# Performance work log

Measured on AMD Instinct MI355X. Metric: run time of the kernel, lower is better.

Reference implementation:

```python
import jax, jax.numpy as jnp
import numpy as np
import math

B, S, D, H, WIDTH, NHW = 8, 1024, 512, 8, 8, 2
DK = D // H
S2 = S + 2 * WIDTH


def setup_inputs() -> dict:
    key = jax.random.key(0)
    ks = jax.random.split(key, 12)
    sc = 1.0 / math.sqrt(D)
    return {
        "x": jax.random.normal(ks[0], (B, S, D), jnp.float32),
        "l_attn_W": jax.random.normal(ks[1], (4, D, D), jnp.float32) * sc,  # q,k,v,out
        "l_attn_b": jnp.zeros((4, D), jnp.float32),
        "r_attn_W": jax.random.normal(ks[2], (4, D, D), jnp.float32) * sc,
        "r_attn_b": jnp.zeros((4, D), jnp.float32),
        "left_pad": jax.random.normal(ks[3], (WIDTH, D), jnp.float32) * sc,
        "right_pad": jax.random.normal(ks[4], (WIDTH, D), jnp.float32) * sc,
        "left_w": jax.random.normal(ks[5], (WIDTH + 1,), jnp.float32),
        "right_w": jax.random.normal(ks[6], (WIDTH + 1,), jnp.float32),
        "l_hw_W": jax.random.normal(ks[7], (NHW, D, 2 * D), jnp.float32) * sc,
        "l_hw_b": jnp.zeros((NHW, 2 * D), jnp.float32),
        "r_hw_W": jax.random.normal(ks[8], (NHW, D, 2 * D), jnp.float32) * sc,
        "r_hw_b": jnp.zeros((NHW, 2 * D), jnp.float32),
    }


def _mha(x, W, b, mask):
    # x: [B, S2, D]; W: [4, D, D]; mask: [1, S2, S2] bool (True = keep)
    q = (x @ W[0] + b[0]).reshape(B, S2, H, DK)
    k = (x @ W[1] + b[1]).reshape(B, S2, H, DK)
    v = (x @ W[2] + b[2]).reshape(B, S2, H, DK)
    scores = jnp.einsum('bihd,bjhd->bhij', q, k) / math.sqrt(DK)
    scores = jnp.where(mask[:, None], scores, jnp.float32(-1e9))
    p = jax.nn.softmax(scores, axis=-1)
    o = jnp.einsum('bhij,bjhd->bihd', p, v).reshape(B, S2, D)
    return o @ W[3] + b[3]


def _highway(x, Ws, bs):
    # AllenNLP-style Highway: projected -> [nonlinear | gate]
    for i in range(NHW):
        proj = x @ Ws[i] + bs[i]
        nl = jax.nn.relu(proj[..., :D])
        g = jax.nn.sigmoid(proj[..., D:])
        x = g * x + (1.0 - g) * nl
    return x


def reference(x, l_attn_W, l_attn_b, r_attn_W, r_attn_b, left_pad, right_pad,
              left_w, right_w, l_hw_W, l_hw_b, r_hw_W, r_hw_b):
    new_in = jnp.concatenate([
        jnp.broadcast_to(left_pad, (B, WIDTH, D)), x,
        jnp.broadcast_to(right_pad, (B, WIDTH, D))], axis=1)  # [B, S2, D]
    idx = jnp.arange(S2)
    diff = idx[:, None] - idx[None, :]
    lmask = ((diff >= 0) & (diff <= WIDTH + 1))[None]          # attend to [i-width-1, i]
    rmask = ((diff <= 0) & (diff >= -(WIDTH + 1)))[None]       # attend to [i, i+width+1]
    nl_attn = _mha(new_in, l_attn_W, l_attn_b, lmask)
    nr_attn = _mha(new_in, r_attn_W, r_attn_b, rmask)
    left_out = nl_attn[:, WIDTH:WIDTH + S, :]   # position end = start + width
    right_out = nr_attn[:, WIDTH:WIDTH + S, :]
    # relative-position weighted sliding windows (vectorized over all steps)
    lrel = sum(left_w[j] * new_in[:, j:j + S, :] for j in range(WIDTH + 1))
    rrel = sum(right_w[j] * new_in[:, WIDTH + j:WIDTH + j + S, :] for j in range(WIDTH + 1))
    left_out = _highway(left_out + lrel, l_hw_W, l_hw_b)
    right_out = _highway(right_out + rrel, r_hw_W, r_hw_b)
    out = jnp.concatenate([left_out, right_out], axis=-1)  # [B, S, 2D]
    return out[None]  # [1, B, S, 2D] matching torch stack layout
```

## Files before the change

kernel.cpp:

```cpp
#include <hip/hip_runtime.h>


#define B_ 8
#define S_ 1024
#define D_ 512
#define H_ 8
#define DK_ 64
#define WIDTH_ 8
#define S2_ 1040
#define NHW_ 2

typedef short bf16x8 __attribute__((ext_vector_type(8)));
typedef float f32x4 __attribute__((ext_vector_type(4)));

__device__ __forceinline__ float us2f(unsigned short u) {
  union { unsigned int i; float f; } c; c.i = ((unsigned int)u) << 16; return c.f;
}
__device__ __forceinline__ unsigned short f2us(float f) {
  union { float f; unsigned int i; } c; c.f = f;
  unsigned int x = c.i;
  return (unsigned short)((x + 0x7fffu + ((x >> 16) & 1u)) >> 16);
}
__device__ __forceinline__ unsigned int pack2(float a, float b) {
  return (unsigned int)f2us(a) | ((unsigned int)f2us(b) << 16);
}
__device__ __forceinline__ void async16(const void* g, void* l) {
  __builtin_amdgcn_global_load_lds(
      (const __attribute__((address_space(1))) void*)g,
      (__attribute__((address_space(3))) void*)l, 16, 0, 0);
}
__device__ __forceinline__ void unpack8(uint4 u, float* f) {
  unsigned int w[4] = {u.x, u.y, u.z, u.w};
  #pragma unroll
  for (int c = 0; c < 4; ++c) {
    union { unsigned int i; float g; } lo, hi;
    lo.i = w[c] << 16;
    hi.i = w[c] & 0xffff0000u;
    f[2 * c] = lo.g;
    f[2 * c + 1] = hi.g;
  }
}

__global__ __launch_bounds__(256) void k_prep(
    const float* __restrict__ x,
    const float* __restrict__ lpad, const float* __restrict__ rpad,
    const float* __restrict__ lW, const float* __restrict__ rW,
    const float* __restrict__ lb, const float* __restrict__ rb,
    const float* __restrict__ lhwW, const float* __restrict__ rhwW,
    unsigned short* __restrict__ WTall, unsigned short* __restrict__ WTp,
    unsigned short* __restrict__ hWT,
    unsigned short* __restrict__ nin, float* __restrict__ qkvbias)
{
  __shared__ float tile[32][33];
  const size_t DD = (size_t)D_ * D_;
  int bx = blockIdx.x;
  int tx = threadIdx.x & 31, ty = threadIdx.x >> 5;

  if (bx < 2048) {
    int sl = bx >> 8, rem = bx & 255;
    int side = sl >> 2, slice = sl & 3;
    int c0 = (rem & 15) * 32, r0 = (rem >> 4) * 32;
    const float* src = (side ? rW : lW) + (size_t)slice * DD;
    unsigned short* dst = (slice < 3) ? WTall + (size_t)(side * 3 + slice) * DD
                                      : WTp + (size_t)side * DD;
    #pragma unroll
    for (int i = 0; i < 4; ++i)
      tile[ty + i * 8][tx] = src[(size_t)(r0 + ty + i * 8) * D_ + c0 + tx];
    __syncthreads();
    #pragma unroll
    for (int i = 0; i < 4; ++i)
      dst[(size_t)(c0 + ty + i * 8) * D_ + r0 + tx] = f2us(tile[tx][ty + i * 8]);
    return;
  }
  if (bx < 4096) {
    int idx = bx - 2048;
    int sl = idx >> 9, rem = idx & 511;
    int c0 = (rem & 31) * 32, r0 = (rem >> 5) * 32;
    const float* src = ((sl >> 1) ? rhwW : lhwW) + (size_t)(sl & 1) * 512 * 1024;
    unsigned short* dst = hWT + (size_t)sl * 1024 * 512;
    #pragma unroll
    for (int i = 0; i < 4; ++i)
      tile[ty + i * 8][tx] = src[(size_t)(r0 + ty + i * 8) * 1024 + c0 + tx];
    __syncthreads();
    #pragma unroll
    for (int i = 0; i < 4; ++i) {
      int c = c0 + ty + i * 8;
      int q = (2 * ((c & 511) >> 4) + (c >= 512 ? 1 : 0)) * 16 + (c & 15);
      dst[(size_t)q * 512 + r0 + tx] = f2us(tile[tx][ty + i * 8]);
    }
    return;
  }
  int gid = (bx - 4096) * 256 + threadIdx.x;
  const int NTH = B_ * S2_ * 64;
  if (gid >= NTH) {
    int t = gid - NTH;
    if (t < 1536) qkvbias[t] = lb[t];
    else if (t < 3072) qkvbias[t] = rb[t - 1536];
    return;
  }
  int c8 = (gid & 63) << 3;
  int row = gid >> 6;
  int b = row / S2_;
  int t = row - b * S2_;
  const float* src;
  if (t < WIDTH_)            src = lpad + (size_t)t * D_ + c8;
  else if (t >= S_ + WIDTH_) src = rpad + (size_t)(t - S_ - WIDTH_) * D_ + c8;
  else                       src = x + ((size_t)b * S_ + (t - WIDTH_)) * D_ + c8;
  float4 a = *reinterpret_cast<const float4*>(src);
  float4 c = *reinterpret_cast<const float4*>(src + 4);
  uint4 o;
  o.x = pack2(a.x, a.y); o.y = pack2(a.z, a.w);
  o.z = pack2(c.x, c.y); o.w = pack2(c.z, c.w);
  *reinterpret_cast<uint4*>(nin + (size_t)row * D_ + c8) = o;
}

__global__ __launch_bounds__(256) void k_gemm_mfma(
    const unsigned short* __restrict__ A,
    const unsigned short* __restrict__ BT,
    const float* __restrict__ bias,
    unsigned short* __restrict__ C,
    int M, int N, int K)
{
  __shared__ unsigned short As[128 * 64];
  __shared__ unsigned short Bs[128 * 64];

  const int tid = threadIdx.x;
  const int w = tid >> 6;
  const int l = tid & 63;
  const int bm = blockIdx.y * 128;
  const int bn = blockIdx.x * 128;
  const int wrow = (w >> 1) * 64;
  const int wcol = (w & 1) * 64;

  const int lr = l >> 3;
  const int sk = (((l & 7) ^ lr) & 7) * 8;
  const unsigned short* Ap = A + (size_t)(bm + w * 8 + lr) * K + sk;
  const unsigned short* Bp = BT + (size_t)(bn + w * 8 + lr) * K + sk;
  unsigned short* lA = &As[w * 512];
  unsigned short* lB = &Bs[w * 512];
  const size_t K32 = (size_t)32 * K;

  const int fl = l & 15;
  const int fq = l >> 4;
  const int fx = fl & 7;

  f32x4 acc[4][4];
  #pragma unroll
  for (int mi = 0; mi < 4; ++mi)
    #pragma unroll
    for (int ni = 0; ni < 4; ++ni) acc[mi][ni] = (f32x4){0.f, 0.f, 0.f, 0.f};

  for (int k0 = 0; k0 < K; k0 += 64) {
    #pragma unroll
    for (int r = 0; r < 4; ++r) {
      async16(Ap + k0 + r * K32, lA + r * 2048);
      async16(Bp + k0 + r * K32, lB + r * 2048);
    }
    __syncthreads();
    #pragma unroll
    for (int s = 0; s < 2; ++s) {
      bf16x8 af[4], bfr[4];
      #pragma unroll
      for (int mi = 0; mi < 4; ++mi)
        af[mi] = *reinterpret_cast<const bf16x8*>(
            &As[(wrow + mi * 16 + fl) * 64 + (((s * 4 + fq) ^ fx) * 8)]);
      #pragma unroll
      for (int ni = 0; ni < 4; ++ni)
        bfr[ni] = *reinterpret_cast<const bf16x8*>(
            &Bs[(wcol + ni * 16 + fl) * 64 + (((s * 4 + fq) ^ fx) * 8)]);
      #pragma unroll
      for (int mi = 0; mi < 4; ++mi)
        #pragma unroll
        for (int ni = 0; ni < 4; ++ni)
          acc[mi][ni] = __builtin_amdgcn_mfma_f32_16x16x32_bf16(
              af[mi], bfr[ni], acc[mi][ni], 0, 0, 0);
    }
    __syncthreads();
  }

  float bv[4];
  #pragma unroll
  for (int ni = 0; ni < 4; ++ni) bv[ni] = bias[bn + wcol + ni * 16 + fl];

  const int rbase = (l >> 4) * 4;
  #pragma unroll
  for (int mi = 0; mi < 4; ++mi) {
    #pragma unroll
    for (int r = 0; r < 4; ++r) {
      int row = bm + wrow + mi * 16 + rbase + r;
      unsigned short* Cp = C + (size_t)row * N + bn + wcol + fl;
      #pragma unroll
      for (int ni = 0; ni < 4; ++ni)
        Cp[ni * 16] = f2us(acc[mi][ni][r] + bv[ni]);
    }
  }
}

__global__ __launch_bounds__(256) void k_gemm_proj(
    const unsigned short* __restrict__ ctx,
    const unsigned short* __restrict__ WTp,
    const unsigned short* __restrict__ nin,
    const float* __restrict__ lb3, const float* __restrict__ rb3,
    const float* __restrict__ wrel0, const float* __restrict__ wrel1,
    unsigned short* __restrict__ hwx)
{
  __shared__ unsigned short smem[128 * 136];
  unsigned short* As = smem;
  unsigned short* Bs = smem + 8192;
  const int K = 512, N = 512;
  const size_t MS = (size_t)B_ * S_ * D_;

  const int z = blockIdx.z;
  const unsigned short* A = ctx + (size_t)z * MS;
  const unsigned short* BT = WTp + (size_t)z * 512 * 512;
  const float* bias = z ? rb3 : lb3;
  const float* wrel = z ? wrel1 : wrel0;
  const int off = z * WIDTH_;

  const int tid = threadIdx.x;
  const int w = tid >> 6;
  const int l = tid & 63;
  const int bm = blockIdx.y * 128;
  const int bn = blockIdx.x * 128;
  const int wrow = (w >> 1) * 64;
  const int wcol = (w & 1) * 64;

  const int lr = l >> 3;
  const int sk = (((l & 7) ^ lr) & 7) * 8;
  const unsigned short* Ap = A + (size_t)(bm + w * 8 + lr) * K + sk;
  const unsigned short* Bp = BT + (size_t)(bn + w * 8 + lr) * K + sk;
  unsigned short* lA = &As[w * 512];
  unsigned short* lB = &Bs[w * 512];
  const size_t K32 = (size_t)32 * K;

  const int fl = l & 15;
  const int fq = l >> 4;
  const int fx = fl & 7;

  f32x4 acc[4][4];
  #pragma unroll
  for (int mi = 0; mi < 4; ++mi)
    #pragma unroll
    for (int ni = 0; ni < 4; ++ni) acc[mi][ni] = (f32x4){0.f, 0.f, 0.f, 0.f};

  for (int k0 = 0; k0 < K; k0 += 64) {
    #pragma unroll
    for (int r = 0; r < 4; ++r) {
      async16(Ap + k0 + r * K32, lA + r * 2048);
      async16(Bp + k0 + r * K32, lB + r * 2048);
    }
    __syncthreads();
    #pragma unroll
    for (int s = 0; s < 2; ++s) {
      bf16x8 af[4], bfr[4];
      #pragma unroll
      for (int mi = 0; mi < 4; ++mi)
        af[mi] = *reinterpret_cast<const bf16x8*>(
            &As[(wrow + mi * 16 + fl) * 64 + (((s * 4 + fq) ^ fx) * 8)]);
      #pragma unroll
      for (int ni = 0; ni < 4; ++ni)
        bfr[ni] = *reinterpret_cast<const bf16x8*>(
            &Bs[(wcol + ni * 16 + fl) * 64 + (((s * 4 + fq) ^ fx) * 8)]);
      #pragma unroll
      for (int mi = 0; mi < 4; ++mi)
        #pragma unroll
        for (int ni = 0; ni < 4; ++ni)
          acc[mi][ni] = __builtin_amdgcn_mfma_f32_16x16x32_bf16(
              af[mi], bfr[ni], acc[mi][ni], 0, 0, 0);
    }
    __syncthreads();
  }

  float bv[4];
  #pragma unroll
  for (int ni = 0; ni < 4; ++ni) bv[ni] = bias[bn + wcol + ni * 16 + fl];
  const int rbase = (l >> 4) * 4;
  #pragma unroll
  for (int mi = 0; mi < 4; ++mi)
    #pragma unroll
    for (int r = 0; r < 4; ++r)
      #pragma unroll
      for (int ni = 0; ni < 4; ++ni)
        smem[(wrow + mi * 16 + rbase + r) * 136 + wcol + ni * 16 + fl] =
            f2us(acc[mi][ni][r] + bv[ni]);
  __syncthreads();

  const int trow = tid >> 4;
  const int tcol = (tid & 15) * 8;
  const float w0 = wrel[0], w1 = wrel[1], w2 = wrel[2], w3 = wrel[3],
              w4 = wrel[4], w5 = wrel[5], w6 = wrel[6], w7 = wrel[7],
              w8 = wrel[8];
  const float wj[9] = {w0, w1, w2, w3, w4, w5, w6, w7, w8};
  #pragma unroll
  for (int i = 0; i < 8; ++i) {
    int r = trow + i * 16;
    int gr = bm + r;
    int b = gr >> 10, s = gr & (S_ - 1);
    float a8[8];
    unpack8(*reinterpret_cast<const uint4*>(&smem[r * 136 + tcol]), a8);
    const unsigned short* np =
        nin + ((size_t)b * S2_ + off + s) * D_ + bn + tcol;
    #pragma unroll
    for (int j = 0; j < 9; ++j) {
      float nf[8];
      unpack8(*reinterpret_cast<const uint4*>(np + (size_t)j * D_), nf);
      #pragma unroll
      for (int e = 0; e < 8; ++e) a8[e] += wj[j] * nf[e];
    }
    uint4 o;
    o.x = pack2(a8[0], a8[1]); o.y = pack2(a8[2], a8[3]);
    o.z = pack2(a8[4], a8[5]); o.w = pack2(a8[6], a8[7]);
    *reinterpret_cast<uint4*>(
        hwx + (size_t)z * MS + (size_t)gr * D_ + bn + tcol) = o;
  }
}

template <bool FINAL>
__global__ __launch_bounds__(256) void k_gemm_hw(
    const unsigned short* __restrict__ Xsrc,
    const unsigned short* __restrict__ BT, size_t bStrZ,
    const float* __restrict__ bias0, const float* __restrict__ bias1,
    unsigned short* __restrict__ Obf,
    float* __restrict__ Ofp)
{
  __shared__ unsigned short As[128 * 64];
  __shared__ unsigned short Bs[128 * 64];
  const int K = 512;
  const size_t MS = (size_t)B_ * S_ * D_;

  const int z = blockIdx.z;
  const unsigned short* A = Xsrc + (size_t)z * MS;
  BT += (size_t)z * bStrZ;
  const float* bias = z ? bias1 : bias0;

  const int tid = threadIdx.x;
  const int w = tid >> 6;
  const int l = tid & 63;
  const int bm = blockIdx.y * 128;
  const int bn = blockIdx.x * 128;
  const int wrow = (w >> 1) * 64;
  const int wcol = (w & 1) * 64;

  const int lr = l >> 3;
  const int sk = (((l & 7) ^ lr) & 7) * 8;
  const unsigned short* Ap = A + (size_t)(bm + w * 8 + lr) * K + sk;
  const unsigned short* Bp = BT + (size_t)(bn + w * 8 + lr) * K + sk;
  unsigned short* lA = &As[w * 512];
  unsigned short* lB = &Bs[w * 512];
  const size_t K32 = (size_t)32 * K;

  const int fl = l & 15;
  const int fq = l >> 4;
  const int fx = fl & 7;

  f32x4 acc[4][4];
  #pragma unroll
  for (int mi = 0; mi < 4; ++mi)
    #pragma unroll
    for (int ni = 0; ni < 4; ++ni) acc[mi][ni] = (f32x4){0.f, 0.f, 0.f, 0.f};

  for (int k0 = 0; k0 < K; k0 += 64) {
    #pragma unroll
    for (int r = 0; r < 4; ++r) {
      async16(Ap + k0 + r * K32, lA + r * 2048);
      async16(Bp + k0 + r * K32, lB + r * 2048);
    }
    __syncthreads();
    #pragma unroll
    for (int s = 0; s < 2; ++s) {
      bf16x8 af[4], bfr[4];
      #pragma unroll
      for (int mi = 0; mi < 4; ++mi)
        af[mi] = *reinterpret_cast<const bf16x8*>(
            &As[(wrow + mi * 16 + fl) * 64 + (((s * 4 + fq) ^ fx) * 8)]);
      #pragma unroll
      for (int ni = 0; ni < 4; ++ni)
        bfr[ni] = *reinterpret_cast<const bf16x8*>(
            &Bs[(wcol + ni * 16 + fl) * 64 + (((s * 4 + fq) ^ fx) * 8)]);
      #pragma unroll
      for (int mi = 0; mi < 4; ++mi)
        #pragma unroll
        for (int ni = 0; ni < 4; ++ni)
          acc[mi][ni] = __builtin_amdgcn_mfma_f32_16x16x32_bf16(
              af[mi], bfr[ni], acc[mi][ni], 0, 0, 0);
    }
    __syncthreads();
  }

  const int ocb = ((bn + wcol) >> 1) + fl;
  float bnl[2], bg[2];
  #pragma unroll
  for (int p = 0; p < 2; ++p) {
    bnl[p] = bias[ocb + p * 16];
    bg[p]  = bias[512 + ocb + p * 16];
  }

  const int rbase = (l >> 4) * 4;
  #pragma unroll
  for (int mi = 0; mi < 4; ++mi) {
    #pragma unroll
    for (int r = 0; r < 4; ++r) {
      int row = bm + wrow + mi * 16 + rbase + r;
      #pragma unroll
      for (int p = 0; p < 2; ++p) {
        int oc = ocb + p * 16;
        float nl = fmaxf(acc[mi][2 * p][r] + bnl[p], 0.f);
        float g  = 1.f / (1.f + __expf(-(acc[mi][2 * p + 1][r] + bg[p])));
        float xv = us2f(A[(size_t)row * 512 + oc]);
        float res = g * xv + (1.f - g) * nl;
        if (FINAL) Ofp[(size_t)row * 1024 + z * 512 + oc] = res;
        else       Obf[(size_t)z * MS + (size_t)row * 512 + oc] = f2us(res);
      }
    }
  }
}

__global__ __launch_bounds__(256) void k_attn_window(
    const unsigned short* __restrict__ qkv,
    unsigned short* __restrict__ ctx)
{
  int wid = (blockIdx.x * 256 + threadIdx.x) >> 6;
  int lane = threadIdx.x & 63;
  int s = wid & (S_ - 1);
  int b = (wid >> 10) & (B_ - 1);
  int dir = wid >> 13;
  int i = s + WIDTH_;

  const size_t base = (size_t)b * S2_ * 3072 + dir * 1536;
  const int c0 = lane * 8;

  float qf[8];
  unpack8(*reinterpret_cast<const uint4*>(qkv + base + (size_t)i * 3072 + c0), qf);

  float sc[10];
  float mx = -1e30f;
  #pragma unroll
  for (int t = 0; t < 10; ++t) {
    int j = (dir == 0) ? (i - 9 + t) : (i + t);
    float sv = -1e30f;
    if (j >= 0 && j < S2_) {
      float kf[8];
      unpack8(*reinterpret_cast<const uint4*>(
          qkv + base + (size_t)j * 3072 + 512 + c0), kf);
      float p = qf[0] * kf[0];
      #pragma unroll
      for (int e = 1; e < 8; ++e) p += qf[e] * kf[e];
      p += __shfl_xor(p, 1);
      p += __shfl_xor(p, 2);
      p += __shfl_xor(p, 4);
      sv = p * 0.125f;
    }
    sc[t] = sv;
    mx = fmaxf(mx, sv);
  }

  float denom = 0.f;
  #pragma unroll
  for (int t = 0; t < 10; ++t) {
    sc[t] = (sc[t] > -1e29f) ? __expf(sc[t] - mx) : 0.f;
    denom += sc[t];
  }
  float inv = 1.f / denom;

  float acc[8] = {0.f, 0.f, 0.f, 0.f, 0.f, 0.f, 0.f, 0.f};
  #pragma unroll
  for (int t = 0; t < 10; ++t) {
    int j = (dir == 0) ? (i - 9 + t) : (i + t);
    if (j >= 0 && j < S2_) {
      float vf[8];
      unpack8(*reinterpret_cast<const uint4*>(
          qkv + base + (size_t)j * 3072 + 1024 + c0), vf);
      float p = sc[t];
      #pragma unroll
      for (int e = 0; e < 8; ++e) acc[e] += p * vf[e];
    }
  }

  uint4 o;
  o.x = pack2(acc[0] * inv, acc[1] * inv);
  o.y = pack2(acc[2] * inv, acc[3] * inv);
  o.z = pack2(acc[4] * inv, acc[5] * inv);
  o.w = pack2(acc[6] * inv, acc[7] * inv);
  *reinterpret_cast<uint4*>(
      ctx + (((size_t)dir * B_ + b) * S_ + s) * D_ + c0) = o;
}

extern "C" void kernel_launch(void* const* d_in, const int* in_sizes, int n_in,
                              void* d_out, int out_size, void* d_ws, size_t ws_size,
                              hipStream_t stream) {
  const float* x    = (const float*)d_in[0];
  const float* lW   = (const float*)d_in[1];
  const float* lb   = (const float*)d_in[2];
  const float* rW   = (const float*)d_in[3];
  const float* rb   = (const float*)d_in[4];
  const float* lpad = (const float*)d_in[5];
  const float* rpad = (const float*)d_in[6];
  const float* lw   = (const float*)d_in[7];
  const float* rw   = (const float*)d_in[8];
  const float* lhwW = (const float*)d_in[9];
  const float* lhwb = (const float*)d_in[10];
  const float* rhwW = (const float*)d_in[11];
  const float* rhwb = (const float*)d_in[12];
  float* out = (float*)d_out;
  unsigned short* ws = (unsigned short*)d_ws;

  const size_t NIN  = (size_t)B_ * S2_ * D_;
  const size_t NQKV = (size_t)B_ * S2_ * 3072;
  const size_t MS   = (size_t)B_ * S_ * D_;
  const size_t DD   = (size_t)D_ * D_;
  const size_t LHW  = (size_t)1024 * 512;

  unsigned short* nin   = ws;
  unsigned short* qkv   = nin + NIN;
  unsigned short* ctx   = qkv + NQKV;
  unsigned short* hwx   = ctx + 2 * MS;
  unsigned short* hwy   = hwx + 2 * MS;
  unsigned short* WTall = hwy + 2 * MS;
  unsigned short* WTp   = WTall + 6 * DD;
  unsigned short* hWT   = WTp + 2 * DD;
  float* qkvbias        = (float*)(hWT + 4 * LHW);

  k_prep<<<6188, 256, 0, stream>>>(x, lpad, rpad, lW, rW, lb, rb, lhwW, rhwW,
                                   WTall, WTp, hWT, nin, qkvbias);

  const int MQ = B_ * S2_;

  {
    dim3 g(3072 / 128, MQ / 128, 1);
    k_gemm_mfma<<<g, 256, 0, stream>>>(nin, WTall, qkvbias, qkv, MQ, 3072, D_);
  }

  k_attn_window<<<(2 * B_ * S_) / 4, 256, 0, stream>>>(qkv, ctx);

  {
    dim3 g(D_ / 128, (B_ * S_) / 128, 2);
    k_gemm_proj<<<g, 256, 0, stream>>>(ctx, WTp, nin, lb + 3 * D_, rb + 3 * D_,
                                       lw, rw, hwx);
  }

  {
    dim3 g(1024 / 128, (B_ * S_) / 128, 2);
    k_gemm_hw<false><<<g, 256, 0, stream>>>(hwx, hWT, 2 * LHW,
                                            lhwb, rhwb, hwy, nullptr);
    k_gemm_hw<true><<<g, 256, 0, stream>>>(hwy, hWT + LHW, 2 * LHW,
                                           lhwb + 1024, rhwb + 1024,
                                           nullptr, out);
  }
}
```

Before: 243.9 us.

## Fuse all stages into one persistent cooperative kernel with grid syncs

Replaces the six separate kernel launches with a single persistent cooperative kernel. It loops blocks over virtual tiles for each stage (prep, QKV GEMM, window attention, projection, two highway GEMMs) and separates the stages with grid-wide syncs. The goal is to remove launch gaps and tail effects between kernels. The costs are that the grid is capped at 512 blocks (two per CU), which may lower occupancy for the attention and prep stages, and that each grid.sync has its own overhead. A fallback path issues the per-stage kernels if the cooperative launch fails.

```diff
diff --git a/kernel.cpp b/kernel.cpp
--- a/kernel.cpp
+++ b/kernel.cpp
@@ -1,5 +1,8 @@
 #include <hip/hip_runtime.h>
-
+#include <hip/hip_cooperative_groups.h>
+
+
+namespace cg = cooperative_groups;
 
 #define B_ 8
 #define S_ 1024
@@ -41,94 +44,22 @@
   }
 }
 
-__global__ __launch_bounds__(256) void k_prep(
-    const float* __restrict__ x,
-    const float* __restrict__ lpad, const float* __restrict__ rpad,
-    const float* __restrict__ lW, const float* __restrict__ rW,
-    const float* __restrict__ lb, const float* __restrict__ rb,
-    const float* __restrict__ lhwW, const float* __restrict__ rhwW,
-    unsigned short* __restrict__ WTall, unsigned short* __restrict__ WTp,
-    unsigned short* __restrict__ hWT,
-    unsigned short* __restrict__ nin, float* __restrict__ qkvbias)
-{
-  __shared__ float tile[32][33];
-  const size_t DD = (size_t)D_ * D_;
-  int bx = blockIdx.x;
-  int tx = threadIdx.x & 31, ty = threadIdx.x >> 5;
-
-  if (bx < 2048) {
-    int sl = bx >> 8, rem = bx & 255;
-    int side = sl >> 2, slice = sl & 3;
-    int c0 = (rem & 15) * 32, r0 = (rem >> 4) * 32;
-    const float* src = (side ? rW : lW) + (size_t)slice * DD;
-    unsigned short* dst = (slice < 3) ? WTall + (size_t)(side * 3 + slice) * DD
-                                      : WTp + (size_t)side * DD;
-    #pragma unroll
-    for (int i = 0; i < 4; ++i)
-      tile[ty + i * 8][tx] = src[(size_t)(r0 + ty + i * 8) * D_ + c0 + tx];
-    __syncthreads();
-    #pragma unroll
-    for (int i = 0; i < 4; ++i)
-      dst[(size_t)(c0 + ty + i * 8) * D_ + r0 + tx] = f2us(tile[tx][ty + i * 8]);
-    return;
-  }
-  if (bx < 4096) {
-    int idx = bx - 2048;
-    int sl = idx >> 9, rem = idx & 511;
-    int c0 = (rem & 31) * 32, r0 = (rem >> 5) * 32;
-    const float* src = ((sl >> 1) ? rhwW : lhwW) + (size_t)(sl & 1) * 512 * 1024;
-    unsigned short* dst = hWT + (size_t)sl * 1024 * 512;
-    #pragma unroll
-    for (int i = 0; i < 4; ++i)
-      tile[ty + i * 8][tx] = src[(size_t)(r0 + ty + i * 8) * 1024 + c0 + tx];
-    __syncthreads();
-    #pragma unroll
-    for (int i = 0; i < 4; ++i) {
-      int c = c0 + ty + i * 8;
-      int q = (2 * ((c & 511) >> 4) + (c >= 512 ? 1 : 0)) * 16 + (c & 15);
-      dst[(size_t)q * 512 + r0 + tx] = f2us(tile[tx][ty + i * 8]);
-    }
-    return;
-  }
-  int gid = (bx - 4096) * 256 + threadIdx.x;
-  const int NTH = B_ * S2_ * 64;
-  if (gid >= NTH) {
-    int t = gid - NTH;
-    if (t < 1536) qkvbias[t] = lb[t];
-    else if (t < 3072) qkvbias[t] = rb[t - 1536];
-    return;
-  }
-  int c8 = (gid & 63) << 3;
-  int row = gid >> 6;
-  int b = row / S2_;
-  int t = row - b * S2_;
-  const float* src;
-  if (t < WIDTH_)            src = lpad + (size_t)t * D_ + c8;
-  else if (t >= S_ + WIDTH_) src = rpad + (size_t)(t - S_ - WIDTH_) * D_ + c8;
-  else                       src = x + ((size_t)b * S_ + (t - WIDTH_)) * D_ + c8;
-  float4 a = *reinterpret_cast<const float4*>(src);
-  float4 c = *reinterpret_cast<const float4*>(src + 4);
-  uint4 o;
-  o.x = pack2(a.x, a.y); o.y = pack2(a.z, a.w);
-  o.z = pack2(c.x, c.y); o.w = pack2(c.z, c.w);
-  *reinterpret_cast<uint4*>(nin + (size_t)row * D_ + c8) = o;
-}
-
-__global__ __launch_bounds__(256) void k_gemm_mfma(
-    const unsigned short* __restrict__ A,
-    const unsigned short* __restrict__ BT,
-    const float* __restrict__ bias,
-    unsigned short* __restrict__ C,
-    int M, int N, int K)
-{
-  __shared__ unsigned short As[128 * 64];
-  __shared__ unsigned short Bs[128 * 64];
-
-  const int tid = threadIdx.x;
+struct Params {
+  const float *x, *lpad, *rpad, *lW, *rW, *lb, *rb, *lhwW, *rhwW,
+              *lhwb, *rhwb, *lw, *rw;
+  float* out;
+  unsigned short *nin, *qkv, *ctx, *hwx, *hwy, *WTall, *WTp, *hWT;
+  float* qkvbias;
+};
+
+__device__ __forceinline__ void kloop512(
+    const unsigned short* __restrict__ A, const unsigned short* __restrict__ BT,
+    int bm, int bn, int tid, unsigned short* As, unsigned short* Bs,
+    f32x4 acc[4][4])
+{
+  const int K = 512;
   const int w = tid >> 6;
   const int l = tid & 63;
-  const int bm = blockIdx.y * 128;
-  const int bn = blockIdx.x * 128;
   const int wrow = (w >> 1) * 64;
   const int wcol = (w & 1) * 64;
 
@@ -144,7 +75,6 @@
   const int fq = l >> 4;
   const int fx = fl & 7;
 
-  f32x4 acc[4][4];
   #pragma unroll
   for (int mi = 0; mi < 4; ++mi)
     #pragma unroll
@@ -177,18 +107,98 @@
     }
     __syncthreads();
   }
+}
+
+__device__ __forceinline__ void prep_block(
+    int bx, int tid, const Params& p, unsigned short* smemu)
+{
+  float (*tile)[33] = reinterpret_cast<float (*)[33]>(smemu);
+  const size_t DD = (size_t)D_ * D_;
+  int tx = tid & 31, ty = tid >> 5;
+
+  if (bx < 2048) {
+    int sl = bx >> 8, rem = bx & 255;
+    int side = sl >> 2, slice = sl & 3;
+    int c0 = (rem & 15) * 32, r0 = (rem >> 4) * 32;
+    const float* src = (side ? p.rW : p.lW) + (size_t)slice * DD;
+    unsigned short* dst = (slice < 3)
+        ? p.WTall + (size_t)(side * 3 + slice) * DD
+        : p.WTp + (size_t)side * DD;
+    #pragma unroll
+    for (int i = 0; i < 4; ++i)
+      tile[ty + i * 8][tx] = src[(size_t)(r0 + ty + i * 8) * D_ + c0 + tx];
+    __syncthreads();
+    #pragma unroll
+    for (int i = 0; i < 4; ++i)
+      dst[(size_t)(c0 + ty + i * 8) * D_ + r0 + tx] = f2us(tile[tx][ty + i * 8]);
+    __syncthreads();
+  } else if (bx < 4096) {
+    int idx = bx - 2048;
+    int sl = idx >> 9, rem = idx & 511;
+    int c0 = (rem & 31) * 32, r0 = (rem >> 5) * 32;
+    const float* src = ((sl >> 1) ? p.rhwW : p.lhwW) + (size_t)(sl & 1) * 512 * 1024;
+    unsigned short* dst = p.hWT + (size_t)sl * 1024 * 512;
+    #pragma unroll
+    for (int i = 0; i < 4; ++i)
+      tile[ty + i * 8][tx] = src[(size_t)(r0 + ty + i * 8) * 1024 + c0 + tx];
+    __syncthreads();
+    #pragma unroll
+    for (int i = 0; i < 4; ++i) {
+      int c = c0 + ty + i * 8;
+      int q = (2 * ((c & 511) >> 4) + (c >= 512 ? 1 : 0)) * 16 + (c & 15);
+      dst[(size_t)q * 512 + r0 + tx] = f2us(tile[tx][ty + i * 8]);
+    }
+    __syncthreads();
+  } else {
+    int gid = (bx - 4096) * 256 + tid;
+    const int NTH = B_ * S2_ * 64;
+    if (gid >= NTH) {
+      int t = gid - NTH;
+      if (t < 1536) p.qkvbias[t] = p.lb[t];
+      else if (t < 3072) p.qkvbias[t] = p.rb[t - 1536];
+    } else {
+      int c8 = (gid & 63) << 3;
+      int row = gid >> 6;
+      int b = row / S2_;
+      int t = row - b * S2_;
+      const float* src;
+      if (t < WIDTH_)            src = p.lpad + (size_t)t * D_ + c8;
+      else if (t >= S_ + WIDTH_) src = p.rpad + (size_t)(t - S_ - WIDTH_) * D_ + c8;
+      else                       src = p.x + ((size_t)b * S_ + (t - WIDTH_)) * D_ + c8;
+      float4 a = *reinterpret_cast<const float4*>(src);
+      float4 c = *reinterpret_cast<const float4*>(src + 4);
+      uint4 o;
+      o.x = pack2(a.x, a.y); o.y = pack2(a.z, a.w);
+      o.z = pack2(c.x, c.y); o.w = pack2(c.z, c.w);
+      *reinterpret_cast<uint4*>(p.nin + (size_t)row * D_ + c8) = o;
+    }
+  }
+}
+
+__device__ __forceinline__ void qkv_tile(
+    int bx, int by, int tid, const Params& p, unsigned short* smemu)
+{
+  const int N = 3072;
+  const int bm = by * 128, bn = bx * 128;
+  const int l = tid & 63;
+  const int w = tid >> 6;
+  const int wrow = (w >> 1) * 64;
+  const int wcol = (w & 1) * 64;
+  const int fl = l & 15;
+
+  f32x4 acc[4][4];
+  kloop512(p.nin, p.WTall, bm, bn, tid, smemu, smemu + 8192, acc);
 
   float bv[4];
   #pragma unroll
-  for (int ni = 0; ni < 4; ++ni) bv[ni] = bias[bn + wcol + ni * 16 + fl];
-
+  for (int ni = 0; ni < 4; ++ni) bv[ni] = p.qkvbias[bn + wcol + ni * 16 + fl];
   const int rbase = (l >> 4) * 4;
   #pragma unroll
   for (int mi = 0; mi < 4; ++mi) {
     #pragma unroll
     for (int r = 0; r < 4; ++r) {
       int row = bm + wrow + mi * 16 + rbase + r;
-      unsigned short* Cp = C + (size_t)row * N + bn + wcol + fl;
+      unsigned short* Cp = p.qkv + (size_t)row * N + bn + wcol + fl;
       #pragma unroll
       for (int ni = 0; ni < 4; ++ni)
         Cp[ni * 16] = f2us(acc[mi][ni][r] + bv[ni]);
@@ -196,231 +206,11 @@
   }
 }
 
-__global__ __launch_bounds__(256) void k_gemm_proj(
-    const unsigned short* __restrict__ ctx,
-    const unsigned short* __restrict__ WTp,
-    const unsigned short* __restrict__ nin,
-    const float* __restrict__ lb3, const float* __restrict__ rb3,
-    const float* __restrict__ wrel0, const float* __restrict__ wrel1,
-    unsigned short* __restrict__ hwx)
-{
-  __shared__ unsigned short smem[128 * 136];
-  unsigned short* As = smem;
-  unsigned short* Bs = smem + 8192;
-  const int K = 512, N = 512;
-  const size_t MS = (size_t)B_ * S_ * D_;
-
-  const int z = blockIdx.z;
-  const unsigned short* A = ctx + (size_t)z * MS;
-  const unsigned short* BT = WTp + (size_t)z * 512 * 512;
-  const float* bias = z ? rb3 : lb3;
-  const float* wrel = z ? wrel1 : wrel0;
-  const int off = z * WIDTH_;
-
-  const int tid = threadIdx.x;
-  const int w = tid >> 6;
-  const int l = tid & 63;
-  const int bm = blockIdx.y * 128;
-  const int bn = blockIdx.x * 128;
-  const int wrow = (w >> 1) * 64;
-  const int wcol = (w & 1) * 64;
-
-  const int lr = l >> 3;
-  const int sk = (((l & 7) ^ lr) & 7) * 8;
-  const unsigned short* Ap = A + (size_t)(bm + w * 8 + lr) * K + sk;
-  const unsigned short* Bp = BT + (size_t)(bn + w * 8 + lr) * K + sk;
-  unsigned short* lA = &As[w * 512];
-  unsigned short* lB = &Bs[w * 512];
-  const size_t K32 = (size_t)32 * K;
-
-  const int fl = l & 15;
-  const int fq = l >> 4;
-  const int fx = fl & 7;
-
-  f32x4 acc[4][4];
-  #pragma unroll
-  for (int mi = 0; mi < 4; ++mi)
-    #pragma unroll
-    for (int ni = 0; ni < 4; ++ni) acc[mi][ni] = (f32x4){0.f, 0.f, 0.f, 0.f};
-
-  for (int k0 = 0; k0 < K; k0 += 64) {
-    #pragma unroll
-    for (int r = 0; r < 4; ++r) {
-      async16(Ap + k0 + r * K32, lA + r * 2048);
-      async16(Bp + k0 + r * K32, lB + r * 2048);
-    }
-    __syncthreads();
-    #pragma unroll
-    for (int s = 0; s < 2; ++s) {
-      bf16x8 af[4], bfr[4];
-      #pragma unroll
-      for (int mi = 0; mi < 4; ++mi)
-        af[mi] = *reinterpret_cast<const bf16x8*>(
-            &As[(wrow + mi * 16 + fl) * 64 + (((s * 4 + fq) ^ fx) * 8)]);
-      #pragma unroll
-      for (int ni = 0; ni < 4; ++ni)
-        bfr[ni] = *reinterpret_cast<const bf16x8*>(
-            &Bs[(wcol + ni * 16 + fl) * 64 + (((s * 4 + fq) ^ fx) * 8)]);
-      #pragma unroll
-      for (int mi = 0; mi < 4; ++mi)
-        #pragma unroll
-        for (int ni = 0; ni < 4; ++ni)
-          acc[mi][ni] = __builtin_amdgcn_mfma_f32_16x16x32_bf16(
-              af[mi], bfr[ni], acc[mi][ni], 0, 0, 0);
-    }
-    __syncthreads();
-  }
-
-  float bv[4];
-  #pragma unroll
-  for (int ni = 0; ni < 4; ++ni) bv[ni] = bias[bn + wcol + ni * 16 + fl];
-  const int rbase = (l >> 4) * 4;
-  #pragma unroll
-  for (int mi = 0; mi < 4; ++mi)
-    #pragma unroll
-    for (int r = 0; r < 4; ++r)
-      #pragma unroll
-      for (int ni = 0; ni < 4; ++ni)
-        smem[(wrow + mi * 16 + rbase + r) * 136 + wcol + ni * 16 + fl] =
-            f2us(acc[mi][ni][r] + bv[ni]);
-  __syncthreads();
-
-  const int trow = tid >> 4;
-  const int tcol = (tid & 15) * 8;
-  const float w0 = wrel[0], w1 = wrel[1], w2 = wrel[2], w3 = wrel[3],
-              w4 = wrel[4], w5 = wrel[5], w6 = wrel[6], w7 = wrel[7],
-              w8 = wrel[8];
-  const float wj[9] = {w0, w1, w2, w3, w4, w5, w6, w7, w8};
-  #pragma unroll
-  for (int i = 0; i < 8; ++i) {
-    int r = trow + i * 16;
-    int gr = bm + r;
-    int b = gr >> 10, s = gr & (S_ - 1);
-    float a8[8];
-    unpack8(*reinterpret_cast<const uint4*>(&smem[r * 136 + tcol]), a8);
-    const unsigned short* np =
-        nin + ((size_t)b * S2_ + off + s) * D_ + bn + tcol;
-    #pragma unroll
-    for (int j = 0; j < 9; ++j) {
-      float nf[8];
-      unpack8(*reinterpret_cast<const uint4*>(np + (size_t)j * D_), nf);
-      #pragma unroll
-      for (int e = 0; e < 8; ++e) a8[e] += wj[j] * nf[e];
-    }
-    uint4 o;
-    o.x = pack2(a8[0], a8[1]); o.y = pack2(a8[2], a8[3]);
-    o.z = pack2(a8[4], a8[5]); o.w = pack2(a8[6], a8[7]);
-    *reinterpret_cast<uint4*>(
-        hwx + (size_t)z * MS + (size_t)gr * D_ + bn + tcol) = o;
-  }
-}
-
-template <bool FINAL>
-__global__ __launch_bounds__(256) void k_gemm_hw(
-    const unsigned short* __restrict__ Xsrc,
-    const unsigned short* __restrict__ BT, size_t bStrZ,
-    const float* __restrict__ bias0, const float* __restrict__ bias1,
-    unsigned short* __restrict__ Obf,
-    float* __restrict__ Ofp)
-{
-  __shared__ unsigned short As[128 * 64];
-  __shared__ unsigned short Bs[128 * 64];
-  const int K = 512;
-  const size_t MS = (size_t)B_ * S_ * D_;
-
-  const int z = blockIdx.z;
-  const unsigned short* A = Xsrc + (size_t)z * MS;
-  BT += (size_t)z * bStrZ;
-  const float* bias = z ? bias1 : bias0;
-
-  const int tid = threadIdx.x;
-  const int w = tid >> 6;
-  const int l = tid & 63;
-  const int bm = blockIdx.y * 128;
-  const int bn = blockIdx.x * 128;
-  const int wrow = (w >> 1) * 64;
-  const int wcol = (w & 1) * 64;
-
-  const int lr = l >> 3;
-  const int sk = (((l & 7) ^ lr) & 7) * 8;
-  const unsigned short* Ap = A + (size_t)(bm + w * 8 + lr) * K + sk;
-  const unsigned short* Bp = BT + (size_t)(bn + w * 8 + lr) * K + sk;
-  unsigned short* lA = &As[w * 512];
-  unsigned short* lB = &Bs[w * 512];
-  const size_t K32 = (size_t)32 * K;
-
-  const int fl = l & 15;
-  const int fq = l >> 4;
-  const int fx = fl & 7;
-
-  f32x4 acc[4][4];
-  #pragma unroll
-  for (int mi = 0; mi < 4; ++mi)
-    #pragma unroll
-    for (int ni = 0; ni < 4; ++ni) acc[mi][ni] = (f32x4){0.f, 0.f, 0.f, 0.f};
-
-  for (int k0 = 0; k0 < K; k0 += 64) {
-    #pragma unroll
-    for (int r = 0; r < 4; ++r) {
-      async16(Ap + k0 + r * K32, lA + r * 2048);
-      async16(Bp + k0 + r * K32, lB + r * 2048);
-    }
-    __syncthreads();
-    #pragma unroll
-    for (int s = 0; s < 2; ++s) {
-      bf16x8 af[4], bfr[4];
-      #pragma unroll
-      for (int mi = 0; mi < 4; ++mi)
-        af[mi] = *reinterpret_cast<const bf16x8*>(
-            &As[(wrow + mi * 16 + fl) * 64 + (((s * 4 + fq) ^ fx) * 8)]);
-      #pragma unroll
-      for (int ni = 0; ni < 4; ++ni)
-        bfr[ni] = *reinterpret_cast<const bf16x8*>(
-            &Bs[(wcol + ni * 16 + fl) * 64 + (((s * 4 + fq) ^ fx) * 8)]);
-      #pragma unroll
-      for (int mi = 0; mi < 4; ++mi)
-        #pragma unroll
-        for (int ni = 0; ni < 4; ++ni)
-          acc[mi][ni] = __builtin_amdgcn_mfma_f32_16x16x32_bf16(
-              af[mi], bfr[ni], acc[mi][ni], 0, 0, 0);
-    }
-    __syncthreads();
-  }
-
-  const int ocb = ((bn + wcol) >> 1) + fl;
-  float bnl[2], bg[2];
-  #pragma unroll
-  for (int p = 0; p < 2; ++p) {
-    bnl[p] = bias[ocb + p * 16];
-    bg[p]  = bias[512 + ocb + p * 16];
-  }
-
-  const int rbase = (l >> 4) * 4;
-  #pragma unroll
-  for (int mi = 0; mi < 4; ++mi) {
-    #pragma unroll
-    for (int r = 0; r < 4; ++r) {
-      int row = bm + wrow + mi * 16 + rbase + r;
-      #pragma unroll
-      for (int p = 0; p < 2; ++p) {
-        int oc = ocb + p * 16;
-        float nl = fmaxf(acc[mi][2 * p][r] + bnl[p], 0.f);
-        float g  = 1.f / (1.f + __expf(-(acc[mi][2 * p + 1][r] + bg[p])));
-        float xv = us2f(A[(size_t)row * 512 + oc]);
-        float res = g * xv + (1.f - g) * nl;
-        if (FINAL) Ofp[(size_t)row * 1024 + z * 512 + oc] = res;
-        else       Obf[(size_t)z * MS + (size_t)row * 512 + oc] = f2us(res);
-      }
-    }
-  }
-}
-
-__global__ __launch_bounds__(256) void k_attn_window(
-    const unsigned short* __restrict__ qkv,
-    unsigned short* __restrict__ ctx)
-{
-  int wid = (blockIdx.x * 256 + threadIdx.x) >> 6;
-  int lane = threadIdx.x & 63;
+__device__ __forceinline__ void attn_block(
+    int bx, int tid, const Params& p)
+{
+  int wid = (bx * 256 + tid) >> 6;
+  int lane = tid & 63;
   int s = wid & (S_ - 1);
   int b = (wid >> 10) & (B_ - 1);
   int dir = wid >> 13;
@@ -430,7 +220,7 @@
   const int c0 = lane * 8;
 
   float qf[8];
-  unpack8(*reinterpret_cast<const uint4*>(qkv + base + (size_t)i * 3072 + c0), qf);
+  unpack8(*reinterpret_cast<const uint4*>(p.qkv + base + (size_t)i * 3072 + c0), qf);
 
   float sc[10];
   float mx = -1e30f;
@@ -441,14 +231,14 @@
     if (j >= 0 && j < S2_) {
       float kf[8];
       unpack8(*reinterpret_cast<const uint4*>(
-          qkv + base + (size_t)j * 3072 + 512 + c0), kf);
-      float p = qf[0] * kf[0];
-      #pragma unroll
-      for (int e = 1; e < 8; ++e) p += qf[e] * kf[e];
-      p += __shfl_xor(p, 1);
-      p += __shfl_xor(p, 2);
-      p += __shfl_xor(p, 4);
-      sv = p * 0.125f;
+          p.qkv + base + (size_t)j * 3072 + 512 + c0), kf);
+      float pr = qf[0] * kf[0];
+      #pragma unroll
+      for (int e = 1; e < 8; ++e) pr += qf[e] * kf[e];
+      pr += __shfl_xor(pr, 1);
+      pr += __shfl_xor(pr, 2);
+      pr += __shfl_xor(pr, 4);
+      sv = pr * 0.125f;
     }
     sc[t] = sv;
     mx = fmaxf(mx, sv);
@@ -469,10 +259,10 @@
     if (j >= 0 && j < S2_) {
       float vf[8];
       unpack8(*reinterpret_cast<const uint4*>(
-          qkv + base + (size_t)j * 3072 + 1024 + c0), vf);
-      float p = sc[t];
-      #pragma unroll
-      for (int e = 0; e < 8; ++e) acc[e] += p * vf[e];
+          p.qkv + base + (size_t)j * 3072 + 1024 + c0), vf);
+      float pr = sc[t];
+      #pragma unroll
+      for (int e = 0; e < 8; ++e) acc[e] += pr * vf[e];
     }
   }
 
@@ -482,26 +272,167 @@
   o.z = pack2(acc[4] * inv, acc[5] * inv);
   o.w = pack2(acc[6] * inv, acc[7] * inv);
   *reinterpret_cast<uint4*>(
-      ctx + (((size_t)dir * B_ + b) * S_ + s) * D_ + c0) = o;
+      p.ctx + (((size_t)dir * B_ + b) * S_ + s) * D_ + c0) = o;
+}
+
+__device__ __forceinline__ void proj_tile(
+    int bx, int by, int z, int tid, const Params& p, unsigned short* smemu)
+{
+  const size_t MS = (size_t)B_ * S_ * D_;
+  const unsigned short* A = p.ctx + (size_t)z * MS;
+  const unsigned short* BT = p.WTp + (size_t)z * 512 * 512;
+  const float* bias = (z ? p.rb : p.lb) + 3 * D_;
+  const float* wrel = z ? p.rw : p.lw;
+  const int off = z * WIDTH_;
+  const int bm = by * 128, bn = bx * 128;
+  const int l = tid & 63;
+  const int w = tid >> 6;
+  const int wrow = (w >> 1) * 64;
+  const int wcol = (w & 1) * 64;
+  const int fl = l & 15;
+
+  f32x4 acc[4][4];
+  kloop512(A, BT, bm, bn, tid, smemu, smemu + 8192, acc);
+
+  float bv[4];
+  #pragma unroll
+  for (int ni = 0; ni < 4; ++ni) bv[ni] = bias[bn + wcol + ni * 16 + fl];
+  const int rbase = (l >> 4) * 4;
+  #pragma unroll
+  for (int mi = 0; mi < 4; ++mi)
+    #pragma unroll
+    for (int r = 0; r < 4; ++r)
+      #pragma unroll
+      for (int ni = 0; ni < 4; ++ni)
+        smemu[(wrow + mi * 16 + rbase + r) * 128 + wcol + ni * 16 + fl] =
+            f2us(acc[mi][ni][r] + bv[ni]);
+  __syncthreads();
+
+  const int trow = tid >> 4;
+  const int tcol = (tid & 15) * 8;
+  float wj[9];
+  #pragma unroll
+  for (int j = 0; j < 9; ++j) wj[j] = wrel[j];
+  #pragma unroll
+  for (int i = 0; i < 8; ++i) {
+    int r = trow + i * 16;
+    int gr = bm + r;
+    int b = gr >> 10, s = gr & (S_ - 1);
+    float a8[8];
+    unpack8(*reinterpret_cast<const uint4*>(&smemu[r * 128 + tcol]), a8);
+    const unsigned short* np =
+        p.nin + ((size_t)b * S2_ + off + s) * D_ + bn + tcol;
+    #pragma unroll
+    for (int j = 0; j < 9; ++j) {
+      float nf[8];
+      unpack8(*reinterpret_cast<const uint4*>(np + (size_t)j * D_), nf);
+      #pragma unroll
+      for (int e = 0; e < 8; ++e) a8[e] += wj[j] * nf[e];
+    }
+    uint4 o;
+    o.x = pack2(a8[0], a8[1]); o.y = pack2(a8[2], a8[3]);
+    o.z = pack2(a8[4], a8[5]); o.w = pack2(a8[6], a8[7]);
+    *reinterpret_cast<uint4*>(
+        p.hwx + (size_t)z * MS + (size_t)gr * D_ + bn + tcol) = o;
+  }
+  __syncthreads();
+}
+
+template <bool FINAL>
+__device__ __forceinline__ void hw_tile(
+    int bx, int by, int z, int tid, const Params& p, unsigned short* smemu)
+{
+  const size_t MS = (size_t)B_ * S_ * D_;
+  const size_t LHW = (size_t)1024 * 512;
+  const unsigned short* A = (FINAL ? p.hwy : p.hwx) + (size_t)z * MS;
+  const unsigned short* BT = p.hWT + (size_t)z * 2 * LHW + (FINAL ? LHW : 0);
+  const float* bias = (z ? p.rhwb : p.lhwb) + (FINAL ? 1024 : 0);
+  const int bm = by * 128, bn = bx * 128;
+  const int l = tid & 63;
+  const int w = tid >> 6;
+  const int wcol = (w & 1) * 64;
+  const int wrow = (w >> 1) * 64;
+  const int fl = l & 15;
+
+  f32x4 acc[4][4];
+  kloop512(A, BT, bm, bn, tid, smemu, smemu + 8192, acc);
+
+  const int ocb = ((bn + wcol) >> 1) + fl;
+  float bnl[2], bg[2];
+  #pragma unroll
+  for (int pp = 0; pp < 2; ++pp) {
+    bnl[pp] = bias[ocb + pp * 16];
+    bg[pp]  = bias[512 + ocb + pp * 16];
+  }
+
+  const int rbase = (l >> 4) * 4;
+  #pragma unroll
+  for (int mi = 0; mi < 4; ++mi) {
+    #pragma unroll
+    for (int r = 0; r < 4; ++r) {
+      int row = bm + wrow + mi * 16 + rbase + r;
+      #pragma unroll
+      for (int pp = 0; pp < 2; ++pp) {
+        int oc = ocb + pp * 16;
+        float nl = fmaxf(acc[mi][2 * pp][r] + bnl[pp], 0.f);
+        float g  = 1.f / (1.f + __expf(-(acc[mi][2 * pp + 1][r] + bg[pp])));
+        float xv = us2f(A[(size_t)row * 512 + oc]);
+        float res = g * xv + (1.f - g) * nl;
+        if (FINAL) p.out[(size_t)row * 1024 + z * 512 + oc] = res;
+        else       p.hwy[(size_t)z * MS + (size_t)row * 512 + oc] = f2us(res);
+      }
+    }
+  }
+}
+
+__global__ __launch_bounds__(256, 2) void k_mega(Params p)
+{
+  __shared__ unsigned short smem[16384];
+  cg::grid_group grid = cg::this_grid();
+  const int tid = threadIdx.x;
+  const int bid = blockIdx.x;
+  const int nb = gridDim.x;
+
+  for (int vb = bid; vb < 6188; vb += nb) prep_block(vb, tid, p, smem);
+  grid.sync();
+  for (int t = bid; t < 1560; t += nb) qkv_tile(t % 24, t / 24, tid, p, smem);
+  grid.sync();
+  for (int vb = bid; vb < 4096; vb += nb) attn_block(vb, tid, p);
+  grid.sync();
+  for (int t = bid; t < 512; t += nb)
+    proj_tile(t & 3, (t >> 2) & 63, t >> 8, tid, p, smem);
+  grid.sync();
+  for (int t = bid; t < 1024; t += nb)
+    hw_tile<false>(t & 7, (t >> 3) & 63, t >> 9, tid, p, smem);
+  grid.sync();
+  for (int t = bid; t < 1024; t += nb)
+    hw_tile<true>(t & 7, (t >> 3) & 63, t >> 9, tid, p, smem);
+}
+
+__global__ __launch_bounds__(256) void k_prep_f(Params p) {
+  __shared__ unsigned short smem[4224];
+  prep_block(blockIdx.x, threadIdx.x, p, smem);
+}
+__global__ __launch_bounds__(256) void k_qkv_f(Params p) {
+  __shared__ unsigned short smem[16384];
+  qkv_tile(blockIdx.x, blockIdx.y, threadIdx.x, p, smem);
+}
+__global__ __launch_bounds__(256) void k_attn_f(Params p) {
+  attn_block(blockIdx.x, threadIdx.x, p);
+}
+__global__ __launch_bounds__(256) void k_proj_f(Params p) {
+  __shared__ unsigned short smem[16384];
+  proj_tile(blockIdx.x, blockIdx.y, blockIdx.z, threadIdx.x, p, smem);
+}
+template <bool FINAL>
+__global__ __launch_bounds__(256) void k_hw_f(Params p) {
+  __shared__ unsigned short smem[16384];
+  hw_tile<FINAL>(blockIdx.x, blockIdx.y, blockIdx.z, threadIdx.x, p, smem);
 }
 
 extern "C" void kernel_launch(void* const* d_in, const int* in_sizes, int n_in,
                               void* d_out, int out_size, void* d_ws, size_t ws_size,
                               hipStream_t stream) {
-  const float* x    = (const float*)d_in[0];
-  const float* lW   = (const float*)d_in[1];
-  const float* lb   = (const float*)d_in[2];
-  const float* rW   = (const float*)d_in[3];
-  const float* rb   = (const float*)d_in[4];
-  const float* lpad = (const float*)d_in[5];
-  const float* rpad = (const float*)d_in[6];
-  const float* lw   = (const float*)d_in[7];
-  const float* rw   = (const float*)d_in[8];
-  const float* lhwW = (const float*)d_in[9];
-  const float* lhwb = (const float*)d_in[10];
-  const float* rhwW = (const float*)d_in[11];
-  const float* rhwb = (const float*)d_in[12];
-  float* out = (float*)d_out;
   unsigned short* ws = (unsigned short*)d_ws;
 
   const size_t NIN  = (size_t)B_ * S2_ * D_;
@@ -510,40 +441,54 @@
   const size_t DD   = (size_t)D_ * D_;
   const size_t LHW  = (size_t)1024 * 512;
 
-  unsigned short* nin   = ws;
-  unsigned short* qkv   = nin + NIN;
-  unsigned short* ctx   = qkv + NQKV;
-  unsigned short* hwx   = ctx + 2 * MS;
-  unsigned short* hwy   = hwx + 2 * MS;
-  unsigned short* WTall = hwy + 2 * MS;
-  unsigned short* WTp   = WTall + 6 * DD;
-  unsigned short* hWT   = WTp + 2 * DD;
-  float* qkvbias        = (float*)(hWT + 4 * LHW);
-
-  k_prep<<<6188, 256, 0, stream>>>(x, lpad, rpad, lW, rW, lb, rb, lhwW, rhwW,
-                                   WTall, WTp, hWT, nin, qkvbias);
-
-  const int MQ = B_ * S2_;
-
-  {
-    dim3 g(3072 / 128, MQ / 128, 1);
-    k_gemm_mfma<<<g, 256, 0, stream>>>(nin, WTall, qkvbias, qkv, MQ, 3072, D_);
-  }
-
-  k_attn_window<<<(2 * B_ * S_) / 4, 256, 0, stream>>>(qkv, ctx);
-
-  {
-    dim3 g(D_ / 128, (B_ * S_) / 128, 2);
-    k_gemm_proj<<<g, 256, 0, stream>>>(ctx, WTp, nin, lb + 3 * D_, rb + 3 * D_,
-                                       lw, rw, hwx);
-  }
-
-  {
-    dim3 g(1024 / 128, (B_ * S_) / 128, 2);
-    k_gemm_hw<false><<<g, 256, 0, stream>>>(hwx, hWT, 2 * LHW,
-                                            lhwb, rhwb, hwy, nullptr);
-    k_gemm_hw<true><<<g, 256, 0, stream>>>(hwy, hWT + LHW, 2 * LHW,
-                                           lhwb + 1024, rhwb + 1024,
-                                           nullptr, out);
-  }
-}
+  Params p;
+  p.x    = (const float*)d_in[0];
+  p.lW   = (const float*)d_in[1];
+  p.lb   = (const float*)d_in[2];
+  p.rW   = (const float*)d_in[3];
+  p.rb   = (const float*)d_in[4];
+  p.lpad = (const float*)d_in[5];
+  p.rpad = (const float*)d_in[6];
+  p.lw   = (const float*)d_in[7];
+  p.rw   = (const float*)d_in[8];
+  p.lhwW = (const float*)d_in[9];
+  p.lhwb = (const float*)d_in[10];
+  p.rhwW = (const float*)d_in[11];
+  p.rhwb = (const float*)d_in[12];
+  p.out  = (float*)d_out;
+
+  p.nin   = ws;
+  p.qkv   = p.nin + NIN;
+  p.ctx   = p.qkv + NQKV;
+  p.hwx   = p.ctx + 2 * MS;
+  p.hwy   = p.hwx + 2 * MS;
+  p.WTall = p.hwy + 2 * MS;
+  p.WTp   = p.WTall + 6 * DD;
+  p.hWT   = p.WTp + 2 * DD;
+  p.qkvbias = (float*)(p.hWT + 4 * LHW);
+
+  int occ = 0;
+  hipError_t qe = hipOccupancyMaxActiveBlocksPerMultiprocessor(
+      &occ, k_mega, 256, 0);
+  int grid = 0;
+  if (qe == hipSuccess && occ > 0) {
+    grid = occ * 256;
+    if (grid > 512) grid = 512;
+  }
+
+  hipError_t le = hipErrorUnknown;
+  if (grid > 0) {
+    void* args[] = {&p};
+    le = hipLaunchCooperativeKernel((const void*)k_mega, dim3(grid), dim3(256),
+                                    args, 0, stream);
+  }
+
+  if (le != hipSuccess) {
+    k_prep_f<<<6188, 256, 0, stream>>>(p);
+    k_qkv_f<<<dim3(24, 65), 256, 0, stream>>>(p);
+    k_attn_f<<<4096, 256, 0, stream>>>(p);
+    k_proj_f<<<dim3(4, 64, 2), 256, 0, stream>>>(p);
+    k_hw_f<false><<<dim3(8, 64, 2), 256, 0, stream>>>(p);
+    k_hw_f<true><<<dim3(8, 64, 2), 256, 0, stream>>>(p);
+  }
+}
```

Measured after the change: 512.1 us. 2.1x slower.
